# Performance work log

Measured on AMD Instinct MI355X. Metric: run time of the kernel, lower is better.

Reference implementation:

```python
import jax, jax.numpy as jnp
import numpy as np

B, NQ, S, D = 2, 2048, 2048, 1024
H, HD, OUT = 16, 64, 1024


def setup_inputs() -> dict:
    key = jax.random.key(0)
    ks = jax.random.split(key, 8)
    scale = 1.0 / np.sqrt(D)
    return {
        "queries": jax.random.normal(ks[0], (B, NQ, D), jnp.float32),
        "keys": jax.random.normal(ks[1], (B, S, D), jnp.float32),
        "values": jax.random.normal(ks[2], (B, S, D), jnp.float32),
        "indicators": jax.random.uniform(ks[3], (B, S), jnp.float32),
        "Wq": jax.random.normal(ks[4], (D, H * HD), jnp.float32) * scale,
        "Wk": jax.random.normal(ks[5], (D, H * HD), jnp.float32) * scale,
        "Wv": jax.random.normal(ks[6], (D, H * HD), jnp.float32) * scale,
        "Wo": jax.random.normal(ks[7], (H * HD, OUT), jnp.float32) * scale,
    }


def reference(queries, keys, values, indicators, Wq, Wk, Wv, Wo):
    b, nq, _ = queries.shape
    s = keys.shape[1]
    # projections -> [b, len, H, HD] -> [b, H, len, HD]
    Q = (queries @ Wq).reshape(b, nq, H, HD).transpose(0, 2, 1, 3)
    K = (keys @ Wk).reshape(b, s, H, HD).transpose(0, 2, 1, 3)
    V = (values @ Wv).reshape(b, s, H, HD).transpose(0, 2, 1, 3)
    # scores [b, H, nq, s], softmax over s, THEN multiplicative mask
    scores = jnp.einsum("bhqd,bhkd->bhqk", Q, K) / jnp.sqrt(jnp.float32(HD))
    probs = jax.nn.softmax(scores, axis=-1)
    probs = probs * indicators[:, None, None, :]  # post-softmax mask
    ctx = jnp.einsum("bhqk,bhkd->bhqd", probs, V)
    ctx = ctx.transpose(0, 2, 1, 3).reshape(b, nq, H * HD)
    return ctx @ Wo
```

## Files before the change

### kernel.cpp

```cpp
#include <hip/hip_runtime.h>


typedef float f32x4 __attribute__((ext_vector_type(4)));
typedef __bf16 bf16x8 __attribute__((ext_vector_type(8)));
typedef __bf16 bf16x4 __attribute__((ext_vector_type(4)));

#define DEVINL __device__ __forceinline__

DEVINL void gll16(const void* g, void* l) {
  __builtin_amdgcn_global_load_lds((const __attribute__((address_space(1))) void*)g,
                                   (__attribute__((address_space(3))) void*)l, 16, 0, 0);
}
DEVINL bf16x8 ldfrag(const void* p) { return __builtin_bit_cast(bf16x8, *(const int4*)p); }
DEVINL f32x4 mfma16(bf16x8 a, bf16x8 b, f32x4 c) {
  return __builtin_amdgcn_mfma_f32_16x16x32_bf16(a, b, c, 0, 0, 0);
}

__global__ __launch_bounds__(256) void prep_k(
    const float* __restrict__ q, const float* __restrict__ k,
    const float* __restrict__ v, const float* __restrict__ Wq,
    const float* __restrict__ Wk, const float* __restrict__ Wv,
    const float* __restrict__ Wo, __bf16* __restrict__ qo, __bf16* __restrict__ ko,
    __bf16* __restrict__ vo, __bf16* __restrict__ o0, __bf16* __restrict__ o1,
    __bf16* __restrict__ o2, __bf16* __restrict__ o3) {
  const int bid = blockIdx.x;
  const int t = threadIdx.x;
  if (bid < 12288) {
    int plane = bid >> 12, bx = bid & 4095;
    const float* s = plane == 0 ? q : (plane == 1 ? k : v);
    __bf16* d = plane == 0 ? qo : (plane == 1 ? ko : vo);
    size_t i = ((size_t)bx * 256 + t) * 4;
    float4 f = *(const float4*)(s + i);
    bf16x4 o = {(__bf16)f.x, (__bf16)f.y, (__bf16)f.z, (__bf16)f.w};
    *(bf16x4*)(d + i) = o;
  } else {
    __shared__ float tl[32][33];
    int wid = bid - 12288;
    int z = wid >> 10, x = wid & 31, y = (wid >> 5) & 31;
    const float* W = z == 0 ? Wq : z == 1 ? Wk : z == 2 ? Wv : Wo;
    __bf16* o = z == 0 ? o0 : z == 1 ? o1 : z == 2 ? o2 : o3;
    float scale = z == 0 ? 0.125f * 1.44269504f : 1.0f;
    int c0 = x * 32, r0 = y * 32;
    int tx = t & 31, ty = t >> 5;
#pragma unroll
    for (int rr = 0; rr < 32; rr += 8)
      tl[rr + ty][tx] = W[(size_t)(r0 + rr + ty) * 1024 + c0 + tx];
    __syncthreads();
#pragma unroll
    for (int cc = 0; cc < 32; cc += 8)
      o[(size_t)(c0 + cc + ty) * 1024 + r0 + tx] = (__bf16)(tl[tx][cc + ty] * scale);
  }
}

template <int MT>
DEVINL void gemm_core(const __bf16* __restrict__ A, const __bf16* __restrict__ Bt,
                      int K, int m0, int n0, char* As, char* Bs, f32x4 (&acc)[MT][4],
                      int t) {
  const int lane = t & 63, wv = t >> 6;
  const int li = lane & 15, g = lane >> 4;
  const int wr = wv >> 1, wc = wv & 1;
  const size_t lda = (size_t)K * 2;
  for (int kt = 0; kt < K; kt += 32) {
    if (kt) __syncthreads();
#pragma unroll
    for (int p = 0; p < MT / 2; ++p) {
      int off = p * 4096 + t * 16;
      int row = off >> 6, ch = (off >> 4) & 3;
      int gch = ch ^ ((row >> 1) & 3);
      gll16((const char*)A + (size_t)(m0 + row) * lda + (size_t)kt * 2 + gch * 16,
            As + off);
    }
#pragma unroll
    for (int p = 0; p < 2; ++p) {
      int off = p * 4096 + t * 16;
      int row = off >> 6, ch = (off >> 4) & 3;
      int gch = ch ^ ((row >> 1) & 3);
      gll16((const char*)Bt + (size_t)(n0 + row) * lda + (size_t)kt * 2 + gch * 16,
            Bs + off);
    }
    __syncthreads();
    bf16x8 af[MT], bfr[4];
#pragma unroll
    for (int mt = 0; mt < MT; ++mt) {
      int row = wr * (MT * 16) + mt * 16 + li;
      int gch = g ^ ((row >> 1) & 3);
      af[mt] = ldfrag(As + row * 64 + gch * 16);
    }
#pragma unroll
    for (int nt = 0; nt < 4; ++nt) {
      int row = wc * 64 + nt * 16 + li;
      int gch = g ^ ((row >> 1) & 3);
      bfr[nt] = ldfrag(Bs + row * 64 + gch * 16);
    }
#pragma unroll
    for (int mt = 0; mt < MT; ++mt)
#pragma unroll
      for (int nt = 0; nt < 4; ++nt)
        acc[mt][nt] = mfma16(af[mt], bfr[nt], acc[mt][nt]);
  }
}

__global__ __launch_bounds__(256) void gemm_qkv(
    const __bf16* __restrict__ qb, const __bf16* __restrict__ kb,
    const __bf16* __restrict__ vb, const __bf16* __restrict__ WqT,
    const __bf16* __restrict__ WkT, const __bf16* __restrict__ WvT,
    const float* __restrict__ ind, __bf16* __restrict__ Qp, __bf16* __restrict__ Kp,
    __bf16* __restrict__ Vtp) {
  __shared__ __align__(16) char As[4 * 2048];
  __shared__ __align__(16) char Bs[8192];
  const int z = blockIdx.z;
  const __bf16* A = z == 0 ? qb : z == 1 ? kb : vb;
  const __bf16* Bt = z == 0 ? WqT : z == 1 ? WkT : WvT;
  const int m0 = blockIdx.y * 128, n0 = blockIdx.x * 128;
  f32x4 acc[4][4] = {};
  gemm_core<4>(A, Bt, 1024, m0, n0, As, Bs, acc, threadIdx.x);
  const int lane = threadIdx.x & 63, wv = threadIdx.x >> 6;
  const int li = lane & 15, g = lane >> 4;
  const int wr = wv >> 1, wc = wv & 1;
#pragma unroll
  for (int mt = 0; mt < 4; ++mt)
#pragma unroll
    for (int nt = 0; nt < 4; ++nt) {
      int m = m0 + wr * 64 + mt * 16 + g * 4;
      int n = n0 + wc * 64 + nt * 16 + li;
      if (z < 2) {
        __bf16* Cb = z ? Kp : Qp;
#pragma unroll
        for (int r = 0; r < 4; ++r)
          Cb[(size_t)(m + r) * 1024 + n] = (__bf16)acc[mt][nt][r];
      } else {
        float4 i4 = *(const float4*)(ind + m);
        bf16x4 o = {(__bf16)(acc[mt][nt][0] * i4.x), (__bf16)(acc[mt][nt][1] * i4.y),
                    (__bf16)(acc[mt][nt][2] * i4.z), (__bf16)(acc[mt][nt][3] * i4.w)};
        *(bf16x4*)(Vtp + (size_t)n * 4096 + m) = o;
      }
    }
}

__global__ __launch_bounds__(256) void gemm_out(const __bf16* __restrict__ ctx,
                                                const __bf16* __restrict__ WoT,
                                                float* __restrict__ out) {
  __shared__ __align__(16) char As[2 * 2048];
  __shared__ __align__(16) char Bs[8192];
  const int m0 = blockIdx.y * 64, n0 = blockIdx.x * 128;
  f32x4 acc[2][4] = {};
  gemm_core<2>(ctx, WoT, 1024, m0, n0, As, Bs, acc, threadIdx.x);
  const int lane = threadIdx.x & 63, wv = threadIdx.x >> 6;
  const int li = lane & 15, g = lane >> 4;
  const int wr = wv >> 1, wc = wv & 1;
#pragma unroll
  for (int mt = 0; mt < 2; ++mt)
#pragma unroll
    for (int nt = 0; nt < 4; ++nt) {
      int m = m0 + wr * 32 + mt * 16 + g * 4;
      int n = n0 + wc * 64 + nt * 16 + li;
#pragma unroll
      for (int r = 0; r < 4; ++r) out[(size_t)(m + r) * 1024 + n] = acc[mt][nt][r];
    }
}

__global__ __launch_bounds__(256) void flash_k(const __bf16* __restrict__ Qp,
                                               const __bf16* __restrict__ Kp,
                                               const __bf16* __restrict__ Vt,
                                               __bf16* __restrict__ ctx0,
                                               __bf16* __restrict__ ctx1,
                                               float* __restrict__ pl) {
  __shared__ __align__(16) char smem[35840];
  char* kv = smem;
  char* qps = smem + 16384;
  const int t = threadIdx.x;
  const int lane = t & 63, wv = t >> 6;
  const int li = lane & 15, g = lane >> 4;
  const int sp = blockIdx.x >> 9, rest = blockIdx.x & 511;
  const int qt = rest & 15, h = (rest >> 4) & 15, b = rest >> 8;
  const size_t qrow0 = (size_t)b * 2048 + (size_t)qt * 128;
  __bf16* ctx = sp ? ctx1 : ctx0;
  char* psw = qps + wv * 4864;

#pragma unroll
  for (int p = 0; p < 4; ++p) {
    int off = p * 4096 + t * 16;
    int row = off >> 7, ch = (off >> 4) & 7;
    int gch = ch ^ (row & 7);
    gll16((const char*)Qp + ((qrow0 + row) * 1024 + h * 64) * 2 + gch * 16, qps + off);
  }
  __syncthreads();

  bf16x8 qf[2][2];
#pragma unroll
  for (int nt = 0; nt < 2; ++nt)
#pragma unroll
    for (int ks = 0; ks < 2; ++ks) {
      int row = wv * 32 + nt * 16 + li;
      int gch = (4 * ks + g) ^ (row & 7);
      qf[nt][ks] = ldfrag(qps + row * 128 + gch * 16);
    }

  f32x4 acc[4][2] = {};
  float lsum[2] = {0.0f, 0.0f};

  for (int kt = sp * 16; kt < sp * 16 + 16; ++kt) {
    __syncthreads();
#pragma unroll
    for (int p = 0; p < 2; ++p) {
      int off = p * 4096 + t * 16;
      int row = off >> 7, ch = (off >> 4) & 7;
      int gch = ch ^ (row & 7);
      gll16((const char*)Kp +
                (((size_t)b * 2048 + kt * 64 + row) * 1024 + h * 64) * 2 + gch * 16,
            kv + off);
      gll16((const char*)Vt +
                ((size_t)(h * 64 + row) * 4096 + (size_t)b * 2048 + kt * 64) * 2 +
                gch * 16,
            kv + 8192 + off);
    }
    __syncthreads();

    f32x4 st[4][2] = {};
#pragma unroll
    for (int ks = 0; ks < 2; ++ks)
#pragma unroll
      for (int mt = 0; mt < 4; ++mt) {
        int row = mt * 16 + li;
        int gch = (4 * ks + g) ^ (row & 7);
        bf16x8 kf = ldfrag(kv + row * 128 + gch * 16);
        st[mt][0] = mfma16(kf, qf[0][ks], st[mt][0]);
        st[mt][1] = mfma16(kf, qf[1][ks], st[mt][1]);
      }

#pragma unroll
    for (int nt = 0; nt < 2; ++nt) {
      float rs = 0.0f;
#pragma unroll
      for (int mt = 0; mt < 4; ++mt) {
        float p0 = __builtin_amdgcn_exp2f(st[mt][nt][0]);
        float p1 = __builtin_amdgcn_exp2f(st[mt][nt][1]);
        float p2 = __builtin_amdgcn_exp2f(st[mt][nt][2]);
        float p3 = __builtin_amdgcn_exp2f(st[mt][nt][3]);
        rs += (p0 + p1) + (p2 + p3);
        bf16x4 pv = {(__bf16)p0, (__bf16)p1, (__bf16)p2, (__bf16)p3};
        *(bf16x4*)(psw + (nt * 16 + li) * 152 + mt * 32 + g * 8) = pv;
      }
      lsum[nt] += rs;
    }

#pragma unroll
    for (int kc = 0; kc < 2; ++kc) {
      bf16x8 pf0 = ldfrag(psw + li * 152 + kc * 64 + g * 16);
      bf16x8 pf1 = ldfrag(psw + (16 + li) * 152 + kc * 64 + g * 16);
#pragma unroll
      for (int mtd = 0; mtd < 4; ++mtd) {
        int row = mtd * 16 + li;
        int gch = (4 * kc + g) ^ (row & 7);
        bf16x8 vf = ldfrag(kv + 8192 + row * 128 + gch * 16);
        acc[mtd][0] = mfma16(vf, pf0, acc[mtd][0]);
        acc[mtd][1] = mfma16(vf, pf1, acc[mtd][1]);
      }
    }
  }

#pragma unroll
  for (int nt = 0; nt < 2; ++nt) {
    float l = lsum[nt];
    l += __shfl_xor(l, 16);
    l += __shfl_xor(l, 32);
    float linv = 1.0f / l;
    size_t qrow = qrow0 + wv * 32 + nt * 16 + li;
    if (g == 0) pl[((size_t)sp * 4096 + qrow) * 16 + h] = l;
#pragma unroll
    for (int mtd = 0; mtd < 4; ++mtd) {
      bf16x4 o = {(__bf16)(acc[mtd][nt][0] * linv), (__bf16)(acc[mtd][nt][1] * linv),
                  (__bf16)(acc[mtd][nt][2] * linv), (__bf16)(acc[mtd][nt][3] * linv)};
      *(bf16x4*)(ctx + qrow * 1024 + h * 64 + mtd * 16 + g * 4) = o;
    }
  }
}

__global__ __launch_bounds__(256) void combine_k(const __bf16* __restrict__ c0,
                                                 const __bf16* __restrict__ c1,
                                                 const float* __restrict__ pl,
                                                 __bf16* __restrict__ ctx) {
  size_t e = ((size_t)blockIdx.x * 256 + threadIdx.x) * 8;
  int qrow = (int)(e >> 10), h = ((int)e & 1023) >> 6;
  float l0 = pl[(size_t)qrow * 16 + h];
  float l1 = pl[(size_t)(4096 + qrow) * 16 + h];
  float w = 1.0f / (l0 + l1);
  float w0 = l0 * w, w1 = l1 * w;
  bf16x8 a = *(const bf16x8*)(c0 + e);
  bf16x8 b = *(const bf16x8*)(c1 + e);
  bf16x8 o;
#pragma unroll
  for (int i = 0; i < 8; ++i) o[i] = (__bf16)((float)a[i] * w0 + (float)b[i] * w1);
  *(bf16x8*)(ctx + e) = o;
}

extern "C" void kernel_launch(void* const* d_in, const int* in_sizes, int n_in,
                              void* d_out, int out_size, void* d_ws, size_t ws_size,
                              hipStream_t stream) {
  const float* q = (const float*)d_in[0];
  const float* k = (const float*)d_in[1];
  const float* v = (const float*)d_in[2];
  const float* ind = (const float*)d_in[3];
  const float* Wq = (const float*)d_in[4];
  const float* Wk = (const float*)d_in[5];
  const float* Wv = (const float*)d_in[6];
  const float* Wo = (const float*)d_in[7];
  char* ws = (char*)d_ws;
  const size_t MB = 1024 * 1024;
  __bf16* qb = (__bf16*)(ws + 0);
  __bf16* kb = (__bf16*)(ws + 8 * MB);
  __bf16* vb = (__bf16*)(ws + 16 * MB);
  __bf16* WqT = (__bf16*)(ws + 24 * MB);
  __bf16* WkT = (__bf16*)(ws + 26 * MB);
  __bf16* WvT = (__bf16*)(ws + 28 * MB);
  __bf16* WoT = (__bf16*)(ws + 30 * MB);
  __bf16* Qp = (__bf16*)(ws + 32 * MB);
  __bf16* Kp = (__bf16*)(ws + 40 * MB);
  __bf16* Vtp = (__bf16*)(ws + 48 * MB);
  __bf16* ctx0 = (__bf16*)(ws + 0);
  __bf16* ctx1 = (__bf16*)(ws + 8 * MB);
  __bf16* ctx = (__bf16*)(ws + 16 * MB);
  float* pl = (float*)(ws + 24 * MB);
  float* out = (float*)d_out;

  prep_k<<<dim3(16384), 256, 0, stream>>>(q, k, v, Wq, Wk, Wv, Wo, qb, kb, vb, WqT,
                                          WkT, WvT, WoT);
  gemm_qkv<<<dim3(8, 32, 3), 256, 0, stream>>>(qb, kb, vb, WqT, WkT, WvT, ind, Qp, Kp,
                                               Vtp);
  flash_k<<<dim3(1024), 256, 0, stream>>>(Qp, Kp, Vtp, ctx0, ctx1, pl);
  combine_k<<<dim3(2048), 256, 0, stream>>>(ctx0, ctx1, pl, ctx);
  gemm_out<<<dim3(8, 64), 256, 0, stream>>>(ctx, WoT, out);
}
```

Baseline: 238.9 us.

## Split flash KV range three ways and pass probabilities via permlane swaps

The flash kernel now splits each (batch, head, q-tile) over three uneven KV ranges instead of two, launching 1536 blocks, and the combine kernel merges three partial contexts. The probability tile is no longer written to and reread from LDS. It is packed to bf16 in registers and rearranged into MFMA operand layout with v_permlane32/16_swap, cutting LDS traffic and shared memory size so more blocks fit per CU. The cost is extra partial-context traffic and combine work, and the final ctx buffer moves to offset 48MB, reusing the Vt region.

```diff
diff --git a/kernel.cpp b/kernel.cpp
--- a/kernel.cpp
+++ b/kernel.cpp
@@ -14,6 +14,21 @@
 DEVINL bf16x8 ldfrag(const void* p) { return __builtin_bit_cast(bf16x8, *(const int4*)p); }
 DEVINL f32x4 mfma16(bf16x8 a, bf16x8 b, f32x4 c) {
   return __builtin_amdgcn_mfma_f32_16x16x32_bf16(a, b, c, 0, 0, 0);
+}
+DEVINL unsigned cvtpk(float a, float b) {
+  union {
+    __bf16 h[2];
+    unsigned u;
+  } r;
+  r.h[0] = (__bf16)a;
+  r.h[1] = (__bf16)b;
+  return r.u;
+}
+DEVINL void swap32(unsigned& a, unsigned& b) {
+  asm("v_permlane32_swap_b32 %0, %1" : "+v"(a), "+v"(b));
+}
+DEVINL void swap16(unsigned& a, unsigned& b) {
+  asm("v_permlane16_swap_b32 %0, %1" : "+v"(a), "+v"(b));
 }
 
 __global__ __launch_bounds__(256) void prep_k(
@@ -159,30 +174,27 @@
     }
 }
 
-__global__ __launch_bounds__(256) void flash_k(const __bf16* __restrict__ Qp,
-                                               const __bf16* __restrict__ Kp,
-                                               const __bf16* __restrict__ Vt,
-                                               __bf16* __restrict__ ctx0,
-                                               __bf16* __restrict__ ctx1,
-                                               float* __restrict__ pl) {
-  __shared__ __align__(16) char smem[35840];
+__global__ __launch_bounds__(256) void flash_k(
+    const __bf16* __restrict__ Qp, const __bf16* __restrict__ Kp,
+    const __bf16* __restrict__ Vt, __bf16* __restrict__ ctx0,
+    __bf16* __restrict__ ctx1, __bf16* __restrict__ ctx2, float* __restrict__ pl) {
+  __shared__ __align__(16) char smem[16384];
   char* kv = smem;
-  char* qps = smem + 16384;
   const int t = threadIdx.x;
   const int lane = t & 63, wv = t >> 6;
   const int li = lane & 15, g = lane >> 4;
   const int sp = blockIdx.x >> 9, rest = blockIdx.x & 511;
   const int qt = rest & 15, h = (rest >> 4) & 15, b = rest >> 8;
+  const int kt0 = (sp * 32) / 3, kt1 = (sp * 32 + 32) / 3;
   const size_t qrow0 = (size_t)b * 2048 + (size_t)qt * 128;
-  __bf16* ctx = sp ? ctx1 : ctx0;
-  char* psw = qps + wv * 4864;
+  __bf16* ctx = sp == 0 ? ctx0 : (sp == 1 ? ctx1 : ctx2);
 
 #pragma unroll
   for (int p = 0; p < 4; ++p) {
     int off = p * 4096 + t * 16;
     int row = off >> 7, ch = (off >> 4) & 7;
     int gch = ch ^ (row & 7);
-    gll16((const char*)Qp + ((qrow0 + row) * 1024 + h * 64) * 2 + gch * 16, qps + off);
+    gll16((const char*)Qp + ((qrow0 + row) * 1024 + h * 64) * 2 + gch * 16, smem + off);
   }
   __syncthreads();
 
@@ -193,13 +205,13 @@
     for (int ks = 0; ks < 2; ++ks) {
       int row = wv * 32 + nt * 16 + li;
       int gch = (4 * ks + g) ^ (row & 7);
-      qf[nt][ks] = ldfrag(qps + row * 128 + gch * 16);
+      qf[nt][ks] = ldfrag(smem + row * 128 + gch * 16);
     }
 
   f32x4 acc[4][2] = {};
   float lsum[2] = {0.0f, 0.0f};
 
-  for (int kt = sp * 16; kt < sp * 16 + 16; ++kt) {
+  for (int kt = kt0; kt < kt1; ++kt) {
     __syncthreads();
 #pragma unroll
     for (int p = 0; p < 2; ++p) {
@@ -216,38 +228,52 @@
     }
     __syncthreads();
 
-    f32x4 st[4][2] = {};
-#pragma unroll
-    for (int ks = 0; ks < 2; ++ks)
-#pragma unroll
-      for (int mt = 0; mt < 4; ++mt) {
-        int row = mt * 16 + li;
+    unsigned pk[4][2][2];
+#pragma unroll
+    for (int mt = 0; mt < 4; ++mt) {
+      f32x4 st0 = {}, st1 = {};
+      int row = mt * 16 + li;
+#pragma unroll
+      for (int ks = 0; ks < 2; ++ks) {
         int gch = (4 * ks + g) ^ (row & 7);
         bf16x8 kf = ldfrag(kv + row * 128 + gch * 16);
-        st[mt][0] = mfma16(kf, qf[0][ks], st[mt][0]);
-        st[mt][1] = mfma16(kf, qf[1][ks], st[mt][1]);
+        st0 = mfma16(kf, qf[0][ks], st0);
+        st1 = mfma16(kf, qf[1][ks], st1);
       }
-
-#pragma unroll
-    for (int nt = 0; nt < 2; ++nt) {
-      float rs = 0.0f;
-#pragma unroll
-      for (int mt = 0; mt < 4; ++mt) {
-        float p0 = __builtin_amdgcn_exp2f(st[mt][nt][0]);
-        float p1 = __builtin_amdgcn_exp2f(st[mt][nt][1]);
-        float p2 = __builtin_amdgcn_exp2f(st[mt][nt][2]);
-        float p3 = __builtin_amdgcn_exp2f(st[mt][nt][3]);
-        rs += (p0 + p1) + (p2 + p3);
-        bf16x4 pv = {(__bf16)p0, (__bf16)p1, (__bf16)p2, (__bf16)p3};
-        *(bf16x4*)(psw + (nt * 16 + li) * 152 + mt * 32 + g * 8) = pv;
-      }
-      lsum[nt] += rs;
+      float p0 = __builtin_amdgcn_exp2f(st0[0]);
+      float p1 = __builtin_amdgcn_exp2f(st0[1]);
+      float p2 = __builtin_amdgcn_exp2f(st0[2]);
+      float p3 = __builtin_amdgcn_exp2f(st0[3]);
+      lsum[0] += (p0 + p1) + (p2 + p3);
+      pk[mt][0][0] = cvtpk(p0, p1);
+      pk[mt][0][1] = cvtpk(p2, p3);
+      p0 = __builtin_amdgcn_exp2f(st1[0]);
+      p1 = __builtin_amdgcn_exp2f(st1[1]);
+      p2 = __builtin_amdgcn_exp2f(st1[2]);
+      p3 = __builtin_amdgcn_exp2f(st1[3]);
+      lsum[1] += (p0 + p1) + (p2 + p3);
+      pk[mt][1][0] = cvtpk(p0, p1);
+      pk[mt][1][1] = cvtpk(p2, p3);
     }
 
 #pragma unroll
     for (int kc = 0; kc < 2; ++kc) {
-      bf16x8 pf0 = ldfrag(psw + li * 152 + kc * 64 + g * 16);
-      bf16x8 pf1 = ldfrag(psw + (16 + li) * 152 + kc * 64 + g * 16);
+      unsigned a00 = pk[2 * kc][0][0], b00 = pk[2 * kc + 1][0][0];
+      unsigned a01 = pk[2 * kc][0][1], b01 = pk[2 * kc + 1][0][1];
+      unsigned a10 = pk[2 * kc][1][0], b10 = pk[2 * kc + 1][1][0];
+      unsigned a11 = pk[2 * kc][1][1], b11 = pk[2 * kc + 1][1][1];
+      swap32(a00, b00);
+      swap16(a00, b00);
+      swap32(a01, b01);
+      swap16(a01, b01);
+      swap32(a10, b10);
+      swap16(a10, b10);
+      swap32(a11, b11);
+      swap16(a11, b11);
+      uint4 u0 = {a00, a01, b00, b01};
+      uint4 u1 = {a10, a11, b10, b11};
+      bf16x8 pf0 = __builtin_bit_cast(bf16x8, u0);
+      bf16x8 pf1 = __builtin_bit_cast(bf16x8, u1);
 #pragma unroll
       for (int mtd = 0; mtd < 4; ++mtd) {
         int row = mtd * 16 + li;
@@ -278,19 +304,23 @@
 
 __global__ __launch_bounds__(256) void combine_k(const __bf16* __restrict__ c0,
                                                  const __bf16* __restrict__ c1,
+                                                 const __bf16* __restrict__ c2,
                                                  const float* __restrict__ pl,
                                                  __bf16* __restrict__ ctx) {
   size_t e = ((size_t)blockIdx.x * 256 + threadIdx.x) * 8;
   int qrow = (int)(e >> 10), h = ((int)e & 1023) >> 6;
   float l0 = pl[(size_t)qrow * 16 + h];
   float l1 = pl[(size_t)(4096 + qrow) * 16 + h];
-  float w = 1.0f / (l0 + l1);
-  float w0 = l0 * w, w1 = l1 * w;
+  float l2 = pl[(size_t)(8192 + qrow) * 16 + h];
+  float w = 1.0f / (l0 + l1 + l2);
+  float w0 = l0 * w, w1 = l1 * w, w2 = l2 * w;
   bf16x8 a = *(const bf16x8*)(c0 + e);
   bf16x8 b = *(const bf16x8*)(c1 + e);
+  bf16x8 c = *(const bf16x8*)(c2 + e);
   bf16x8 o;
 #pragma unroll
-  for (int i = 0; i < 8; ++i) o[i] = (__bf16)((float)a[i] * w0 + (float)b[i] * w1);
+  for (int i = 0; i < 8; ++i)
+    o[i] = (__bf16)((float)a[i] * w0 + (float)b[i] * w1 + (float)c[i] * w2);
   *(bf16x8*)(ctx + e) = o;
 }
 
@@ -319,15 +349,16 @@
   __bf16* Vtp = (__bf16*)(ws + 48 * MB);
   __bf16* ctx0 = (__bf16*)(ws + 0);
   __bf16* ctx1 = (__bf16*)(ws + 8 * MB);
-  __bf16* ctx = (__bf16*)(ws + 16 * MB);
+  __bf16* ctx2 = (__bf16*)(ws + 16 * MB);
   float* pl = (float*)(ws + 24 * MB);
+  __bf16* ctx = (__bf16*)(ws + 48 * MB);
   float* out = (float*)d_out;
 
   prep_k<<<dim3(16384), 256, 0, stream>>>(q, k, v, Wq, Wk, Wv, Wo, qb, kb, vb, WqT,
                                           WkT, WvT, WoT);
   gemm_qkv<<<dim3(8, 32, 3), 256, 0, stream>>>(qb, kb, vb, WqT, WkT, WvT, ind, Qp, Kp,
                                                Vtp);
-  flash_k<<<dim3(1024), 256, 0, stream>>>(Qp, Kp, Vtp, ctx0, ctx1, pl);
-  combine_k<<<dim3(2048), 256, 0, stream>>>(ctx0, ctx1, pl, ctx);
+  flash_k<<<dim3(1536), 256, 0, stream>>>(Qp, Kp, Vtp, ctx0, ctx1, ctx2, pl);
+  combine_k<<<dim3(2048), 256, 0, stream>>>(ctx0, ctx1, ctx2, pl, ctx);
   gemm_out<<<dim3(8, 64), 256, 0, stream>>>(ctx, WoT, out);
 }
```

Result: faster. 228.2 us (-4.5%).
